# Performance work log

Measured on AMD Instinct MI355X. Metric: run time of the kernel, lower is better.

Reference implementation:

```python
import jax, jax.numpy as jnp
import numpy as np

E = 512   # embed_dim
S = 16    # stat_dim
B = 2048  # batch
K = 64    # neighbors


def setup_inputs() -> dict:
    key = jax.random.key(0)
    ks = jax.random.split(key, 12)
    std_s1 = 1.0 / np.sqrt(3 * E + S)
    std_s2 = 1.0 / np.sqrt(E)
    std_p1 = 1.0 / np.sqrt(E + S)
    return {
        "query": jax.random.normal(ks[0], (B, E), jnp.float32),
        "condition": jax.random.normal(ks[1], (B, E), jnp.float32),
        "neighbors": jax.random.normal(ks[2], (B, K, E), jnp.float32),
        "neighbor_stats": jax.random.uniform(ks[3], (B, K, S), jnp.float32),
        # scorer: Linear(3E+S -> E), GELU, Linear(E -> 1)
        "sw1": jax.random.uniform(ks[4], (3 * E + S, E), jnp.float32, -std_s1, std_s1),
        "sb1": jax.random.uniform(ks[5], (E,), jnp.float32, -std_s1, std_s1),
        "sw2": jax.random.uniform(ks[6], (E, 1), jnp.float32, -std_s2, std_s2),
        "sb2": jax.random.uniform(ks[7], (1,), jnp.float32, -std_s2, std_s2),
        "sim_alpha": jnp.float32(1.0),
        # proj: Linear(E+S -> E), GELU, Linear(E -> E)
        "pw1": jax.random.uniform(ks[8], (E + S, E), jnp.float32, -std_p1, std_p1),
        "pb1": jax.random.uniform(ks[9], (E,), jnp.float32, -std_p1, std_p1),
        "pw2": jax.random.uniform(ks[10], (E, E), jnp.float32, -std_s2, std_s2),
        "pb2": jax.random.uniform(ks[11], (E,), jnp.float32, -std_s2, std_s2),
    }


def _gelu(x):
    return jax.nn.gelu(x, approximate=False)  # torch default GELU is exact erf


def reference(query, condition, neighbors, neighbor_stats,
              sw1, sb1, sw2, sb2, sim_alpha, pw1, pb1, pw2, pb2):
    b, k, e = neighbors.shape
    # broadcast query/condition over k and concat -> [B, K, 3E+S]
    q_rep = jnp.broadcast_to(query[:, None, :], (b, k, e))
    c_rep = jnp.broadcast_to(condition[:, None, :], (b, k, e))
    scorer_in = jnp.concatenate([q_rep, c_rep, neighbors, neighbor_stats], axis=-1)
    h = _gelu(scorer_in @ sw1 + sb1)          # dropout is identity in eval
    logits = (h @ sw2 + sb2)[..., 0]           # [B, K]
    sim_scores = neighbor_stats[..., -1]       # stat_dim > 0
    logits = logits + sim_alpha * sim_scores
    attn = jax.nn.softmax(logits, axis=-1)     # [B, K]
    nb_cat = jnp.concatenate([neighbors, neighbor_stats], axis=-1)  # [B, K, E+S]
    mixed = jnp.einsum('bk,bkd->bd', attn, nb_cat)
    out = _gelu(mixed @ pw1 + pb1) @ pw2 + pb2  # [B, E]
    return out, attn
```

## Files before the change

kernel.cpp:

```cpp
#include <hip/hip_runtime.h>

typedef _Float16 half_t;
typedef _Float16 half2_t __attribute__((ext_vector_type(2)));
typedef _Float16 half4_t __attribute__((ext_vector_type(4)));
typedef _Float16 half8_t __attribute__((ext_vector_type(8)));
typedef float floatx4 __attribute__((ext_vector_type(4)));
typedef float floatx16 __attribute__((ext_vector_type(16)));

#define NE 512
#define NS 16
#define NBATCH 2048
#define NK 64
#define AS 552

__device__ __forceinline__ float gelu_erf(float x) {
    float z = x * 0.70710678118654752440f;
    float az2 = z * z;
    float az = __builtin_fabsf(z);
    float t = __builtin_amdgcn_rcpf(__builtin_fmaf(0.3275911f, az, 1.0f));
    float p = __builtin_fmaf(1.061405429f, t, -1.453152027f);
    p = __builtin_fmaf(p, t, 1.421413741f);
    p = __builtin_fmaf(p, t, -0.284496736f);
    p = __builtin_fmaf(p, t, 0.254829592f);
    p = p * t;
    float e = __expf(-az2);
    float erfa = __builtin_fmaf(-p, e, 1.0f);
    unsigned int u = __float_as_uint(erfa) ^ (__float_as_uint(z) & 0x80000000u);
    return 0.5f * x * (1.0f + __uint_as_float(u));
}

__device__ __forceinline__ half4_t cvt4(float4 v) {
    return (half4_t){(half_t)v.x, (half_t)v.y, (half_t)v.z, (half_t)v.w};
}

__device__ __forceinline__ float colreduce16(const float (&x)[16], int lnb) {
    float y[8];
#pragma unroll
    for (int i = 0; i < 8; ++i) {
        float keep = (lnb & 1) ? x[2 * i + 1] : x[2 * i];
        float send = (lnb & 1) ? x[2 * i] : x[2 * i + 1];
        y[i] = keep + __shfl_xor(send, 1, 64);
    }
    float z[4];
#pragma unroll
    for (int i = 0; i < 4; ++i) {
        float keep = (lnb & 2) ? y[2 * i + 1] : y[2 * i];
        float send = (lnb & 2) ? y[2 * i] : y[2 * i + 1];
        z[i] = keep + __shfl_xor(send, 2, 64);
    }
    float u[2];
#pragma unroll
    for (int i = 0; i < 2; ++i) {
        float keep = (lnb & 4) ? z[2 * i + 1] : z[2 * i];
        float send = (lnb & 4) ? z[2 * i] : z[2 * i + 1];
        u[i] = keep + __shfl_xor(send, 4, 64);
    }
    float keep = (lnb & 8) ? u[1] : u[0];
    float send = (lnb & 8) ? u[0] : u[1];
    float v = keep + __shfl_xor(send, 8, 64);
    v += __shfl_xor(v, 16, 64);
    return v;
}

__device__ void pack_w_body(const float* __restrict__ src, half_t* __restrict__ dst,
                            int Ksrc, int t, int nb0, half_t* tile) {
    int tid = threadIdx.x;
#pragma unroll
    for (int i = 0; i < 8; ++i) {
        int idx = tid + i * 256;
        int kk = idx >> 6, np = idx & 63;
        int k = t * 32 + kk;
        float v = (k < Ksrc) ? src[(size_t)k * NE + nb0 + np] : 0.0f;
        tile[kk * 68 + np] = (half_t)v;
    }
    __syncthreads();
#pragma unroll
    for (int i = 0; i < 8; ++i) {
        int idx = tid + i * 256;
        int np = idx >> 5, kk = idx & 31;
        dst[((size_t)t * NE + nb0 + np) * 32 + kk] = tile[kk * 68 + np];
    }
}

__device__ void pack_w32_body(const float* __restrict__ src, half_t* __restrict__ dst,
                              int Ksrc, int t, int nb0, half_t* tile) {
    int tid = threadIdx.x;
#pragma unroll
    for (int i = 0; i < 4; ++i) {
        int idx = tid + i * 256;
        int kk = idx >> 6, n = idx & 63;
        int k = t * 16 + kk;
        float v = (k < Ksrc) ? src[(size_t)k * NE + nb0 + n] : 0.0f;
        tile[kk * 68 + n] = (half_t)v;
    }
    __syncthreads();
    int n = threadIdx.x >> 2, q = threadIdx.x & 3;
    half4_t h = {tile[(q * 4) * 68 + n], tile[(q * 4 + 1) * 68 + n],
                 tile[(q * 4 + 2) * 68 + n], tile[(q * 4 + 3) * 68 + n]};
    *(half4_t*)&dst[((size_t)t * NE + nb0 + n) * 16 + q * 4] = h;
}

__global__ __launch_bounds__(256) void pack_all(
    const float* __restrict__ sw1, const float* __restrict__ pw1,
    const float* __restrict__ pw2, half_t* __restrict__ Wq,
    half_t* __restrict__ Wns, half_t* __restrict__ Wp1, half_t* __restrict__ Wp2) {
    __shared__ half_t tile[32 * 68];
    int bx = blockIdx.x;
    if (bx < 256) {
        pack_w_body(sw1, Wq, 1024, bx >> 3, (bx & 7) * 64, tile);
    } else if (bx < 520) {
        int b2 = bx - 256;
        pack_w32_body(sw1 + (size_t)1024 * NE, Wns, 528, b2 >> 3, (b2 & 7) * 64, tile);
    } else if (bx < 656) {
        int b3 = bx - 520;
        pack_w_body(pw1, Wp1, 528, b3 >> 3, (b3 & 7) * 64, tile);
    } else {
        int b4 = bx - 656;
        pack_w_body(pw2, Wp2, 512, b4 >> 3, (b4 & 7) * 64, tile);
    }
}

__global__ __launch_bounds__(512) void qc_kernel(const float* __restrict__ q,
                                                 const float* __restrict__ c,
                                                 const half_t* __restrict__ Wq,
                                                 const float* __restrict__ sb1,
                                                 float* __restrict__ qcb) {
    constexpr int AS1 = 1032;
    __shared__ __align__(16) half_t A1[16 * AS1];
    int b0 = (blockIdx.x >> 1) * 16;
    int nh = (blockIdx.x & 1) * 256;
    int tid = threadIdx.x;
#pragma unroll
    for (int i = 0; i < 8; ++i) {
        int f = tid + i * 512;
        int row = f >> 8;
        int c4 = f & 255;
        const float* srcp = (c4 < 128) ? (q + (size_t)(b0 + row) * NE + c4 * 4)
                                       : (c + (size_t)(b0 + row) * NE + (c4 - 128) * 4);
        float4 v = *(const float4*)srcp;
        *(half4_t*)&A1[row * AS1 + c4 * 4] = cvt4(v);
    }
    __syncthreads();
    int w = tid >> 6, l = tid & 63, lg = l >> 4, ln = l & 15;
    floatx4 acc[2] = { {0,0,0,0}, {0,0,0,0} };
    for (int t = 0; t < 32; ++t) {
        half8_t a = *(const half8_t*)&A1[ln * AS1 + t * 32 + 8 * lg];
#pragma unroll
        for (int ni = 0; ni < 2; ++ni) {
            int n = nh + w * 32 + ni * 16 + ln;
            half8_t bf = *(const half8_t*)(Wq + ((size_t)t * NE + n) * 32 + 8 * lg);
            acc[ni] = __builtin_amdgcn_mfma_f32_16x16x32_f16(a, bf, acc[ni], 0, 0, 0);
        }
    }
#pragma unroll
    for (int ni = 0; ni < 2; ++ni) {
        int col = nh + w * 32 + ni * 16 + ln;
        float bias = sb1[col];
#pragma unroll
        for (int r = 0; r < 4; ++r) {
            int row = 4 * lg + r;
            qcb[(size_t)(b0 + row) * NE + col] = acc[ni][r] + bias;
        }
    }
}

__global__ __launch_bounds__(512, 4) void main_kernel(
    const float* __restrict__ neighbors, const float* __restrict__ stats,
    const half_t* __restrict__ Wns, const float* __restrict__ qcb,
    const float* __restrict__ sw2, const float* __restrict__ sb2,
    const float* __restrict__ alpha, float* __restrict__ attn_out,
    half_t* __restrict__ mixed) {
    __shared__ __align__(16) half_t A[64 * AS];
    __shared__ float Llds[64][17];
    __shared__ float attn_s[8][64];

    int b = blockIdx.x;
    int tid = threadIdx.x;
    const float* nb = neighbors + (size_t)b * NK * NE;
    const float* st = stats + (size_t)b * NK * NS;

    int r0 = tid >> 5;
    int c4 = tid & 31;
    int w = tid >> 6;
    int l = tid & 63, ln = l & 31, hi = l >> 5;
    const half_t* Abase = A + ln * AS + 8 * hi;
    const half_t* WbA = Wns + ((size_t)(w * 64 + ln)) * 16 + 8 * hi;
    const half_t* WbB = WbA + 32 * 16;

    float4 s0, s1, s2, s3;
    float qvA, wA, qvB, wB;
    half8_t bfA[4], bfB[4];

    {
        float4 p0 = *(const float4*)(nb + (size_t)(r0) * NE + 4 * c4);
        float4 p1 = *(const float4*)(nb + (size_t)(r0 + 16) * NE + 4 * c4);
        float4 p2 = *(const float4*)(nb + (size_t)(r0 + 32) * NE + 4 * c4);
        float4 p3 = *(const float4*)(nb + (size_t)(r0 + 48) * NE + 4 * c4);
        qvA = qcb[(size_t)b * NE + w * 64 + ln];
        wA = sw2[w * 64 + ln];
        qvB = qcb[(size_t)b * NE + w * 64 + 32 + ln];
        wB = sw2[w * 64 + 32 + ln];
#pragma unroll
        for (int s = 0; s < 4; ++s) {
            bfA[s] = *(const half8_t*)(WbA + (size_t)s * 8192);
            bfB[s] = *(const half8_t*)(WbB + (size_t)s * 8192);
        }
        __builtin_amdgcn_sched_barrier(0);
        *(half4_t*)&A[(r0) * AS + 4 * c4] = cvt4(p0);
        *(half4_t*)&A[(r0 + 16) * AS + 4 * c4] = cvt4(p1);
        *(half4_t*)&A[(r0 + 32) * AS + 4 * c4] = cvt4(p2);
        *(half4_t*)&A[(r0 + 48) * AS + 4 * c4] = cvt4(p3);
    }
    asm volatile("s_waitcnt lgkmcnt(0)" ::: "memory");
    __builtin_amdgcn_sched_barrier(0);
    __builtin_amdgcn_s_barrier();
    __builtin_amdgcn_sched_barrier(0);

    floatx16 acc00 = {0,0,0,0,0,0,0,0,0,0,0,0,0,0,0,0};
    floatx16 acc01 = {0,0,0,0,0,0,0,0,0,0,0,0,0,0,0,0};
    floatx16 acc10 = {0,0,0,0,0,0,0,0,0,0,0,0,0,0,0,0};
    floatx16 acc11 = {0,0,0,0,0,0,0,0,0,0,0,0,0,0,0,0};

#pragma unroll 1
    for (int ch = 0; ch < 3; ++ch) {
        s0 = *(const float4*)(nb + (size_t)(r0) * NE + (ch + 1) * 128 + 4 * c4);
        s1 = *(const float4*)(nb + (size_t)(r0 + 16) * NE + (ch + 1) * 128 + 4 * c4);
        s2 = *(const float4*)(nb + (size_t)(r0 + 32) * NE + (ch + 1) * 128 + 4 * c4);
        s3 = *(const float4*)(nb + (size_t)(r0 + 48) * NE + (ch + 1) * 128 + 4 * c4);
        __builtin_amdgcn_sched_barrier(0);
#pragma unroll
        for (int s8 = 0; s8 < 8; ++s8) {
            const int slot = s8 & 3;
            half8_t bA = bfA[slot], bB = bfB[slot];
            bfA[slot] = *(const half8_t*)(WbA + (size_t)(ch * 8 + s8 + 4) * 8192);
            bfB[slot] = *(const half8_t*)(WbB + (size_t)(ch * 8 + s8 + 4) * 8192);
            int col = ch * 128 + s8 * 16;
            half8_t a0 = *(const half8_t*)&Abase[col];
            half8_t a1 = *(const half8_t*)&Abase[32 * AS + col];
            acc00 = __builtin_amdgcn_mfma_f32_32x32x16_f16(a0, bA, acc00, 0, 0, 0);
            acc10 = __builtin_amdgcn_mfma_f32_32x32x16_f16(a1, bA, acc10, 0, 0, 0);
            acc01 = __builtin_amdgcn_mfma_f32_32x32x16_f16(a0, bB, acc01, 0, 0, 0);
            acc11 = __builtin_amdgcn_mfma_f32_32x32x16_f16(a1, bB, acc11, 0, 0, 0);
        }
        __builtin_amdgcn_sched_barrier(0);
        *(half4_t*)&A[(r0) * AS + (ch + 1) * 128 + 4 * c4] = cvt4(s0);
        *(half4_t*)&A[(r0 + 16) * AS + (ch + 1) * 128 + 4 * c4] = cvt4(s1);
        *(half4_t*)&A[(r0 + 32) * AS + (ch + 1) * 128 + 4 * c4] = cvt4(s2);
        *(half4_t*)&A[(r0 + 48) * AS + (ch + 1) * 128 + 4 * c4] = cvt4(s3);
        asm volatile("s_waitcnt lgkmcnt(0)" ::: "memory");
        __builtin_amdgcn_sched_barrier(0);
        __builtin_amdgcn_s_barrier();
        __builtin_amdgcn_sched_barrier(0);
    }

    {
        if (tid < 256)
            s0 = *(const float4*)(st + (tid >> 2) * NS + (tid & 3) * 4);
        __builtin_amdgcn_sched_barrier(0);
#pragma unroll
        for (int s8 = 0; s8 < 8; ++s8) {
            const int slot = s8 & 3;
            half8_t bA = bfA[slot], bB = bfB[slot];
            if (s8 <= 4) {
                bfA[slot] = *(const half8_t*)(WbA + (size_t)(28 + s8) * 8192);
                bfB[slot] = *(const half8_t*)(WbB + (size_t)(28 + s8) * 8192);
            }
            int col = 3 * 128 + s8 * 16;
            half8_t a0 = *(const half8_t*)&Abase[col];
            half8_t a1 = *(const half8_t*)&Abase[32 * AS + col];
            acc00 = __builtin_amdgcn_mfma_f32_32x32x16_f16(a0, bA, acc00, 0, 0, 0);
            acc10 = __builtin_amdgcn_mfma_f32_32x32x16_f16(a1, bA, acc10, 0, 0, 0);
            acc01 = __builtin_amdgcn_mfma_f32_32x32x16_f16(a0, bB, acc01, 0, 0, 0);
            acc11 = __builtin_amdgcn_mfma_f32_32x32x16_f16(a1, bB, acc11, 0, 0, 0);
        }
        __builtin_amdgcn_sched_barrier(0);
        if (tid < 256)
            *(half4_t*)&A[(tid >> 2) * AS + 512 + (tid & 3) * 4] = cvt4(s0);
        asm volatile("s_waitcnt lgkmcnt(0)" ::: "memory");
        __builtin_amdgcn_sched_barrier(0);
        __builtin_amdgcn_s_barrier();
        __builtin_amdgcn_sched_barrier(0);
    }
    {
        half8_t a0 = *(const half8_t*)&Abase[512];
        half8_t a1 = *(const half8_t*)&Abase[32 * AS + 512];
        acc00 = __builtin_amdgcn_mfma_f32_32x32x16_f16(a0, bfA[0], acc00, 0, 0, 0);
        acc10 = __builtin_amdgcn_mfma_f32_32x32x16_f16(a1, bfA[0], acc10, 0, 0, 0);
        acc01 = __builtin_amdgcn_mfma_f32_32x32x16_f16(a0, bfB[0], acc01, 0, 0, 0);
        acc11 = __builtin_amdgcn_mfma_f32_32x32x16_f16(a1, bfB[0], acc11, 0, 0, 0);
    }

    {
        float g0[16];
#pragma unroll
        for (int r = 0; r < 16; ++r) g0[r] = gelu_erf(acc00[r] + qvA) * wA;
        float rA = colreduce16(g0, ln);
#pragma unroll
        for (int r = 0; r < 16; ++r) g0[r] = gelu_erf(acc01[r] + qvB) * wB;
        float rB = colreduce16(g0, ln);
        if (ln < 16) {
            int row = (ln & 3) + 8 * (ln >> 2) + 4 * hi;
            Llds[row][2 * w] = rA;
            Llds[row][2 * w + 1] = rB;
        }
#pragma unroll
        for (int r = 0; r < 16; ++r) g0[r] = gelu_erf(acc10[r] + qvA) * wA;
        rA = colreduce16(g0, ln);
#pragma unroll
        for (int r = 0; r < 16; ++r) g0[r] = gelu_erf(acc11[r] + qvB) * wB;
        rB = colreduce16(g0, ln);
        if (ln < 16) {
            int row = (ln & 3) + 8 * (ln >> 2) + 4 * hi;
            Llds[32 + row][2 * w] = rA;
            Llds[32 + row][2 * w + 1] = rB;
        }
    }
    __syncthreads();

    {
        int k = l;
        float lsum = 0.0f;
#pragma unroll
        for (int j = 0; j < 16; ++j) lsum += Llds[k][j];
        float sim = st[k * NS + (NS - 1)];
        float logit = lsum + sb2[0] + alpha[0] * sim;
        float mx = logit;
#pragma unroll
        for (int m = 1; m < 64; m <<= 1) mx = fmaxf(mx, __shfl_xor(mx, m, 64));
        float e = __expf(logit - mx);
        float s = e;
#pragma unroll
        for (int m = 1; m < 64; m <<= 1) s += __shfl_xor(s, m, 64);
        float at = e / s;
        attn_s[w][k] = at;
        if (w == 0) attn_out[(size_t)b * NK + k] = at;
    }

    if (tid < 264) {
        int c0 = 2 * tid;
        float m0 = 0.0f, m1 = 0.0f;
#pragma unroll 8
        for (int k = 0; k < NK; ++k) {
            half2_t v = *(const half2_t*)&A[k * AS + c0];
            float aw = attn_s[w][k];
            m0 += aw * (float)v[0];
            m1 += aw * (float)v[1];
        }
        *(half2_t*)&mixed[(size_t)b * AS + c0] = (half2_t){(half_t)m0, (half_t)m1};
    } else if (tid < 270) {
        int z = tid - 264;
        half4_t hz = {};
        *(half4_t*)&mixed[(size_t)b * AS + 528 + 4 * z] = hz;
    }
}

__global__ __launch_bounds__(1024) void proj_kernel(
    const half_t* __restrict__ mixedp, const half_t* __restrict__ Wp1,
    const half_t* __restrict__ Wp2, const float* __restrict__ pb1,
    const float* __restrict__ pb2, float* __restrict__ out) {
    constexpr int AS3 = AS;
    __shared__ __align__(16) half_t A1[16 * AS3];
    int b0 = blockIdx.x * 16;
    int tid = threadIdx.x;
    const uint4* src = (const uint4*)(mixedp + (size_t)b0 * AS3);
    for (int i = tid; i < 1104; i += 1024) ((uint4*)A1)[i] = src[i];
    __syncthreads();

    int w = tid >> 6, l = tid & 63, lg = l >> 4, ln = l & 15;
    floatx4 acc[2] = { {0,0,0,0}, {0,0,0,0} };
    for (int t = 0; t < 17; ++t) {
        half8_t a = *(const half8_t*)&A1[ln * AS3 + t * 32 + 8 * lg];
#pragma unroll
        for (int ni = 0; ni < 2; ++ni) {
            int n = w * 32 + ni * 16 + ln;
            half8_t bf = *(const half8_t*)(Wp1 + ((size_t)t * NE + n) * 32 + 8 * lg);
            acc[ni] = __builtin_amdgcn_mfma_f32_16x16x32_f16(a, bf, acc[ni], 0, 0, 0);
        }
    }
    __syncthreads();
#pragma unroll
    for (int ni = 0; ni < 2; ++ni) {
        int col = w * 32 + ni * 16 + ln;
        float bias = pb1[col];
#pragma unroll
        for (int r = 0; r < 4; ++r) {
            int row = 4 * lg + r;
            A1[row * AS3 + col] = (half_t)gelu_erf(acc[ni][r] + bias);
        }
    }
    __syncthreads();
    floatx4 acc2[2] = { {0,0,0,0}, {0,0,0,0} };
    for (int t = 0; t < 16; ++t) {
        half8_t a = *(const half8_t*)&A1[ln * AS3 + t * 32 + 8 * lg];
#pragma unroll
        for (int ni = 0; ni < 2; ++ni) {
            int n = w * 32 + ni * 16 + ln;
            half8_t bf = *(const half8_t*)(Wp2 + ((size_t)t * NE + n) * 32 + 8 * lg);
            acc2[ni] = __builtin_amdgcn_mfma_f32_16x16x32_f16(a, bf, acc2[ni], 0, 0, 0);
        }
    }
#pragma unroll
    for (int ni = 0; ni < 2; ++ni) {
        int col = w * 32 + ni * 16 + ln;
        float bias = pb2[col];
#pragma unroll
        for (int r = 0; r < 4; ++r)
            out[(size_t)(b0 + 4 * lg + r) * NE + col] = acc2[ni][r] + bias;
    }
}

extern "C" void kernel_launch(void* const* d_in, const int* in_sizes, int n_in,
                              void* d_out, int out_size, void* d_ws, size_t ws_size,
                              hipStream_t stream) {
    (void)in_sizes; (void)n_in; (void)out_size; (void)ws_size;
    const float* q     = (const float*)d_in[0];
    const float* c     = (const float*)d_in[1];
    const float* nb    = (const float*)d_in[2];
    const float* st    = (const float*)d_in[3];
    const float* sw1   = (const float*)d_in[4];
    const float* sb1   = (const float*)d_in[5];
    const float* sw2   = (const float*)d_in[6];
    const float* sb2   = (const float*)d_in[7];
    const float* alpha = (const float*)d_in[8];
    const float* pw1   = (const float*)d_in[9];
    const float* pb1   = (const float*)d_in[10];
    const float* pw2   = (const float*)d_in[11];
    const float* pb2   = (const float*)d_in[12];

    char* ws = (char*)d_ws;
    half_t* Wq  = (half_t*)(ws + 0);
    half_t* Wns = (half_t*)(ws + 1048576);
    half_t* Wp1 = (half_t*)(ws + 1605632);
    half_t* Wp2 = (half_t*)(ws + 2162688);
    float*  qcb = (float*)(ws + 2686976);
    half_t* mix = (half_t*)(ws + 6881280);

    float* outp  = (float*)d_out;
    float* attnp = outp + (size_t)NBATCH * NE;

    pack_all<<<784, 256, 0, stream>>>(sw1, pw1, pw2, Wq, Wns, Wp1, Wp2);
    qc_kernel<<<256, 512, 0, stream>>>(q, c, Wq, sb1, qcb);
    main_kernel<<<2048, 512, 0, stream>>>(nb, st, Wns, qcb, sw2, sb2, alpha, attnp, mix);
    proj_kernel<<<128, 1024, 0, stream>>>(mix, Wp1, Wp2, pb1, pb2, outp);
}
```

Baseline: 182.6 us.

## Halve main_kernel block to 4 waves, each covering 128 hidden columns

Restructures main_kernel from 512 threads (8 waves, 64 hidden columns each) to 256 threads (4 waves, 128 columns each). Each wave now reuses every A-fragment LDS read across 8 MFMAs instead of 4, and double-buffers weight fragments in two register sets. Neighbor chunks are prefetched two chunks ahead with wider per-thread loads, and the stats chunk is folded into the main loop. This cuts LDS traffic per MFMA but doubles accumulator registers and lowers launch occupancy, which reduces latency hiding. The mixed-sum tail is redistributed so 256 threads cover 528 columns.

```diff
diff --git a/kernel.cpp b/kernel.cpp
--- a/kernel.cpp
+++ b/kernel.cpp
@@ -60,6 +60,19 @@
     float v = keep + __shfl_xor(send, 8, 64);
     v += __shfl_xor(v, 16, 64);
     return v;
+}
+
+__device__ __forceinline__ void epi_one(const floatx16& acc, float qv, float w2,
+                                        int rowofs, int cg, int ln, int hi,
+                                        float (*Llds)[17]) {
+    float g[16];
+#pragma unroll
+    for (int r = 0; r < 16; ++r) g[r] = gelu_erf(acc[r] + qv) * w2;
+    float rr = colreduce16(g, ln);
+    if (ln < 16) {
+        int row = (ln & 3) + 8 * (ln >> 2) + 4 * hi;
+        Llds[rowofs + row][cg] = rr;
+    }
 }
 
 __device__ void pack_w_body(const float* __restrict__ src, half_t* __restrict__ dst,
@@ -164,7 +177,7 @@
     }
 }
 
-__global__ __launch_bounds__(512, 4) void main_kernel(
+__global__ __launch_bounds__(256, 2) void main_kernel(
     const float* __restrict__ neighbors, const float* __restrict__ stats,
     const half_t* __restrict__ Wns, const float* __restrict__ qcb,
     const float* __restrict__ sw2, const float* __restrict__ sb2,
@@ -172,44 +185,67 @@
     half_t* __restrict__ mixed) {
     __shared__ __align__(16) half_t A[64 * AS];
     __shared__ float Llds[64][17];
-    __shared__ float attn_s[8][64];
+    __shared__ float attn_s[4][64];
 
     int b = blockIdx.x;
     int tid = threadIdx.x;
     const float* nb = neighbors + (size_t)b * NK * NE;
     const float* st = stats + (size_t)b * NK * NS;
 
-    int r0 = tid >> 5;
-    int c4 = tid & 31;
+    int r0 = tid >> 4;
+    int c4 = tid & 15;
     int w = tid >> 6;
     int l = tid & 63, ln = l & 31, hi = l >> 5;
     const half_t* Abase = A + ln * AS + 8 * hi;
-    const half_t* WbA = Wns + ((size_t)(w * 64 + ln)) * 16 + 8 * hi;
-    const half_t* WbB = WbA + 32 * 16;
-
-    float4 s0, s1, s2, s3;
-    float qvA, wA, qvB, wB;
-    half8_t bfA[4], bfB[4];
+    const half_t* Wb = Wns + ((size_t)(w * 128 + ln)) * 16 + 8 * hi;
+
+    float4 s0, s1, s2, s3, s4, s5, s6, s7;
+    float qv0, qv1, qv2, qv3, w20, w21, w22, w23;
+    half8_t bx0, bx1, bx2, bx3, by0, by1, by2, by3;
 
     {
         float4 p0 = *(const float4*)(nb + (size_t)(r0) * NE + 4 * c4);
         float4 p1 = *(const float4*)(nb + (size_t)(r0 + 16) * NE + 4 * c4);
         float4 p2 = *(const float4*)(nb + (size_t)(r0 + 32) * NE + 4 * c4);
         float4 p3 = *(const float4*)(nb + (size_t)(r0 + 48) * NE + 4 * c4);
-        qvA = qcb[(size_t)b * NE + w * 64 + ln];
-        wA = sw2[w * 64 + ln];
-        qvB = qcb[(size_t)b * NE + w * 64 + 32 + ln];
-        wB = sw2[w * 64 + 32 + ln];
-#pragma unroll
-        for (int s = 0; s < 4; ++s) {
-            bfA[s] = *(const half8_t*)(WbA + (size_t)s * 8192);
-            bfB[s] = *(const half8_t*)(WbB + (size_t)s * 8192);
-        }
+        float4 p4 = *(const float4*)(nb + (size_t)(r0) * NE + 64 + 4 * c4);
+        float4 p5 = *(const float4*)(nb + (size_t)(r0 + 16) * NE + 64 + 4 * c4);
+        float4 p6 = *(const float4*)(nb + (size_t)(r0 + 32) * NE + 64 + 4 * c4);
+        float4 p7 = *(const float4*)(nb + (size_t)(r0 + 48) * NE + 64 + 4 * c4);
+        qv0 = qcb[(size_t)b * NE + w * 128 + ln];
+        qv1 = qcb[(size_t)b * NE + w * 128 + 32 + ln];
+        qv2 = qcb[(size_t)b * NE + w * 128 + 64 + ln];
+        qv3 = qcb[(size_t)b * NE + w * 128 + 96 + ln];
+        w20 = sw2[w * 128 + ln];
+        w21 = sw2[w * 128 + 32 + ln];
+        w22 = sw2[w * 128 + 64 + ln];
+        w23 = sw2[w * 128 + 96 + ln];
+        bx0 = *(const half8_t*)(Wb);
+        bx1 = *(const half8_t*)(Wb + 512);
+        bx2 = *(const half8_t*)(Wb + 1024);
+        bx3 = *(const half8_t*)(Wb + 1536);
+        by0 = *(const half8_t*)(Wb + 8192);
+        by1 = *(const half8_t*)(Wb + 8192 + 512);
+        by2 = *(const half8_t*)(Wb + 8192 + 1024);
+        by3 = *(const half8_t*)(Wb + 8192 + 1536);
         __builtin_amdgcn_sched_barrier(0);
         *(half4_t*)&A[(r0) * AS + 4 * c4] = cvt4(p0);
         *(half4_t*)&A[(r0 + 16) * AS + 4 * c4] = cvt4(p1);
         *(half4_t*)&A[(r0 + 32) * AS + 4 * c4] = cvt4(p2);
         *(half4_t*)&A[(r0 + 48) * AS + 4 * c4] = cvt4(p3);
+        *(half4_t*)&A[(r0) * AS + 64 + 4 * c4] = cvt4(p4);
+        *(half4_t*)&A[(r0 + 16) * AS + 64 + 4 * c4] = cvt4(p5);
+        *(half4_t*)&A[(r0 + 32) * AS + 64 + 4 * c4] = cvt4(p6);
+        *(half4_t*)&A[(r0 + 48) * AS + 64 + 4 * c4] = cvt4(p7);
+        __builtin_amdgcn_sched_barrier(0);
+        s0 = *(const float4*)(nb + (size_t)(r0) * NE + 128 + 4 * c4);
+        s1 = *(const float4*)(nb + (size_t)(r0 + 16) * NE + 128 + 4 * c4);
+        s2 = *(const float4*)(nb + (size_t)(r0 + 32) * NE + 128 + 4 * c4);
+        s3 = *(const float4*)(nb + (size_t)(r0 + 48) * NE + 128 + 4 * c4);
+        s4 = *(const float4*)(nb + (size_t)(r0) * NE + 192 + 4 * c4);
+        s5 = *(const float4*)(nb + (size_t)(r0 + 16) * NE + 192 + 4 * c4);
+        s6 = *(const float4*)(nb + (size_t)(r0 + 32) * NE + 192 + 4 * c4);
+        s7 = *(const float4*)(nb + (size_t)(r0 + 48) * NE + 192 + 4 * c4);
     }
     asm volatile("s_waitcnt lgkmcnt(0)" ::: "memory");
     __builtin_amdgcn_sched_barrier(0);
@@ -218,103 +254,112 @@
 
     floatx16 acc00 = {0,0,0,0,0,0,0,0,0,0,0,0,0,0,0,0};
     floatx16 acc01 = {0,0,0,0,0,0,0,0,0,0,0,0,0,0,0,0};
+    floatx16 acc02 = {0,0,0,0,0,0,0,0,0,0,0,0,0,0,0,0};
+    floatx16 acc03 = {0,0,0,0,0,0,0,0,0,0,0,0,0,0,0,0};
     floatx16 acc10 = {0,0,0,0,0,0,0,0,0,0,0,0,0,0,0,0};
     floatx16 acc11 = {0,0,0,0,0,0,0,0,0,0,0,0,0,0,0,0};
+    floatx16 acc12 = {0,0,0,0,0,0,0,0,0,0,0,0,0,0,0,0};
+    floatx16 acc13 = {0,0,0,0,0,0,0,0,0,0,0,0,0,0,0,0};
 
 #pragma unroll 1
-    for (int ch = 0; ch < 3; ++ch) {
-        s0 = *(const float4*)(nb + (size_t)(r0) * NE + (ch + 1) * 128 + 4 * c4);
-        s1 = *(const float4*)(nb + (size_t)(r0 + 16) * NE + (ch + 1) * 128 + 4 * c4);
-        s2 = *(const float4*)(nb + (size_t)(r0 + 32) * NE + (ch + 1) * 128 + 4 * c4);
-        s3 = *(const float4*)(nb + (size_t)(r0 + 48) * NE + (ch + 1) * 128 + 4 * c4);
+    for (int ch = 0; ch < 4; ++ch) {
+#pragma unroll
+        for (int s2i = 0; s2i < 4; ++s2i) {
+            {
+                int te = ch * 8 + 2 * s2i;
+                int col = te * 16;
+                half8_t a0 = *(const half8_t*)&Abase[col];
+                half8_t a1 = *(const half8_t*)&Abase[32 * AS + col];
+                acc00 = __builtin_amdgcn_mfma_f32_32x32x16_f16(a0, bx0, acc00, 0, 0, 0);
+                acc10 = __builtin_amdgcn_mfma_f32_32x32x16_f16(a1, bx0, acc10, 0, 0, 0);
+                acc01 = __builtin_amdgcn_mfma_f32_32x32x16_f16(a0, bx1, acc01, 0, 0, 0);
+                acc11 = __builtin_amdgcn_mfma_f32_32x32x16_f16(a1, bx1, acc11, 0, 0, 0);
+                acc02 = __builtin_amdgcn_mfma_f32_32x32x16_f16(a0, bx2, acc02, 0, 0, 0);
+                acc12 = __builtin_amdgcn_mfma_f32_32x32x16_f16(a1, bx2, acc12, 0, 0, 0);
+                acc03 = __builtin_amdgcn_mfma_f32_32x32x16_f16(a0, bx3, acc03, 0, 0, 0);
+                acc13 = __builtin_amdgcn_mfma_f32_32x32x16_f16(a1, bx3, acc13, 0, 0, 0);
+                int tn = te + 2; if (tn > 32) tn = 32;
+                const half_t* Wt = Wb + (size_t)tn * 8192;
+                bx0 = *(const half8_t*)(Wt);
+                bx1 = *(const half8_t*)(Wt + 512);
+                bx2 = *(const half8_t*)(Wt + 1024);
+                bx3 = *(const half8_t*)(Wt + 1536);
+            }
+            {
+                int to = ch * 8 + 2 * s2i + 1;
+                int col = to * 16;
+                half8_t a0 = *(const half8_t*)&Abase[col];
+                half8_t a1 = *(const half8_t*)&Abase[32 * AS + col];
+                acc00 = __builtin_amdgcn_mfma_f32_32x32x16_f16(a0, by0, acc00, 0, 0, 0);
+                acc10 = __builtin_amdgcn_mfma_f32_32x32x16_f16(a1, by0, acc10, 0, 0, 0);
+                acc01 = __builtin_amdgcn_mfma_f32_32x32x16_f16(a0, by1, acc01, 0, 0, 0);
+                acc11 = __builtin_amdgcn_mfma_f32_32x32x16_f16(a1, by1, acc11, 0, 0, 0);
+                acc02 = __builtin_amdgcn_mfma_f32_32x32x16_f16(a0, by2, acc02, 0, 0, 0);
+                acc12 = __builtin_amdgcn_mfma_f32_32x32x16_f16(a1, by2, acc12, 0, 0, 0);
+                acc03 = __builtin_amdgcn_mfma_f32_32x32x16_f16(a0, by3, acc03, 0, 0, 0);
+                acc13 = __builtin_amdgcn_mfma_f32_32x32x16_f16(a1, by3, acc13, 0, 0, 0);
+                int tn = to + 2; if (tn > 32) tn = 32;
+                const half_t* Wt = Wb + (size_t)tn * 8192;
+                by0 = *(const half8_t*)(Wt);
+                by1 = *(const half8_t*)(Wt + 512);
+                by2 = *(const half8_t*)(Wt + 1024);
+                by3 = *(const half8_t*)(Wt + 1536);
+            }
+        }
         __builtin_amdgcn_sched_barrier(0);
-#pragma unroll
-        for (int s8 = 0; s8 < 8; ++s8) {
-            const int slot = s8 & 3;
-            half8_t bA = bfA[slot], bB = bfB[slot];
-            bfA[slot] = *(const half8_t*)(WbA + (size_t)(ch * 8 + s8 + 4) * 8192);
-            bfB[slot] = *(const half8_t*)(WbB + (size_t)(ch * 8 + s8 + 4) * 8192);
-            int col = ch * 128 + s8 * 16;
-            half8_t a0 = *(const half8_t*)&Abase[col];
-            half8_t a1 = *(const half8_t*)&Abase[32 * AS + col];
-            acc00 = __builtin_amdgcn_mfma_f32_32x32x16_f16(a0, bA, acc00, 0, 0, 0);
-            acc10 = __builtin_amdgcn_mfma_f32_32x32x16_f16(a1, bA, acc10, 0, 0, 0);
-            acc01 = __builtin_amdgcn_mfma_f32_32x32x16_f16(a0, bB, acc01, 0, 0, 0);
-            acc11 = __builtin_amdgcn_mfma_f32_32x32x16_f16(a1, bB, acc11, 0, 0, 0);
-        }
-        __builtin_amdgcn_sched_barrier(0);
-        *(half4_t*)&A[(r0) * AS + (ch + 1) * 128 + 4 * c4] = cvt4(s0);
-        *(half4_t*)&A[(r0 + 16) * AS + (ch + 1) * 128 + 4 * c4] = cvt4(s1);
-        *(half4_t*)&A[(r0 + 32) * AS + (ch + 1) * 128 + 4 * c4] = cvt4(s2);
-        *(half4_t*)&A[(r0 + 48) * AS + (ch + 1) * 128 + 4 * c4] = cvt4(s3);
+        if (ch < 3) {
+            int cb = (ch + 1) * 128;
+            *(half4_t*)&A[(r0) * AS + cb + 4 * c4] = cvt4(s0);
+            *(half4_t*)&A[(r0 + 16) * AS + cb + 4 * c4] = cvt4(s1);
+            *(half4_t*)&A[(r0 + 32) * AS + cb + 4 * c4] = cvt4(s2);
+            *(half4_t*)&A[(r0 + 48) * AS + cb + 4 * c4] = cvt4(s3);
+            *(half4_t*)&A[(r0) * AS + cb + 64 + 4 * c4] = cvt4(s4);
+            *(half4_t*)&A[(r0 + 16) * AS + cb + 64 + 4 * c4] = cvt4(s5);
+            *(half4_t*)&A[(r0 + 32) * AS + cb + 64 + 4 * c4] = cvt4(s6);
+            *(half4_t*)&A[(r0 + 48) * AS + cb + 64 + 4 * c4] = cvt4(s7);
+            __builtin_amdgcn_sched_barrier(0);
+            if (ch < 2) {
+                int nc = (ch + 2) * 128;
+                s0 = *(const float4*)(nb + (size_t)(r0) * NE + nc + 4 * c4);
+                s1 = *(const float4*)(nb + (size_t)(r0 + 16) * NE + nc + 4 * c4);
+                s2 = *(const float4*)(nb + (size_t)(r0 + 32) * NE + nc + 4 * c4);
+                s3 = *(const float4*)(nb + (size_t)(r0 + 48) * NE + nc + 4 * c4);
+                s4 = *(const float4*)(nb + (size_t)(r0) * NE + nc + 64 + 4 * c4);
+                s5 = *(const float4*)(nb + (size_t)(r0 + 16) * NE + nc + 64 + 4 * c4);
+                s6 = *(const float4*)(nb + (size_t)(r0 + 32) * NE + nc + 64 + 4 * c4);
+                s7 = *(const float4*)(nb + (size_t)(r0 + 48) * NE + nc + 64 + 4 * c4);
+            } else {
+                s0 = *(const float4*)(st + (tid >> 2) * NS + (tid & 3) * 4);
+            }
+        } else {
+            *(half4_t*)&A[(tid >> 2) * AS + 512 + (tid & 3) * 4] = cvt4(s0);
+        }
         asm volatile("s_waitcnt lgkmcnt(0)" ::: "memory");
         __builtin_amdgcn_sched_barrier(0);
         __builtin_amdgcn_s_barrier();
         __builtin_amdgcn_sched_barrier(0);
     }
-
-    {
-        if (tid < 256)
-            s0 = *(const float4*)(st + (tid >> 2) * NS + (tid & 3) * 4);
-        __builtin_amdgcn_sched_barrier(0);
-#pragma unroll
-        for (int s8 = 0; s8 < 8; ++s8) {
-            const int slot = s8 & 3;
-            half8_t bA = bfA[slot], bB = bfB[slot];
-            if (s8 <= 4) {
-                bfA[slot] = *(const half8_t*)(WbA + (size_t)(28 + s8) * 8192);
-                bfB[slot] = *(const half8_t*)(WbB + (size_t)(28 + s8) * 8192);
-            }
-            int col = 3 * 128 + s8 * 16;
-            half8_t a0 = *(const half8_t*)&Abase[col];
-            half8_t a1 = *(const half8_t*)&Abase[32 * AS + col];
-            acc00 = __builtin_amdgcn_mfma_f32_32x32x16_f16(a0, bA, acc00, 0, 0, 0);
-            acc10 = __builtin_amdgcn_mfma_f32_32x32x16_f16(a1, bA, acc10, 0, 0, 0);
-            acc01 = __builtin_amdgcn_mfma_f32_32x32x16_f16(a0, bB, acc01, 0, 0, 0);
-            acc11 = __builtin_amdgcn_mfma_f32_32x32x16_f16(a1, bB, acc11, 0, 0, 0);
-        }
-        __builtin_amdgcn_sched_barrier(0);
-        if (tid < 256)
-            *(half4_t*)&A[(tid >> 2) * AS + 512 + (tid & 3) * 4] = cvt4(s0);
-        asm volatile("s_waitcnt lgkmcnt(0)" ::: "memory");
-        __builtin_amdgcn_sched_barrier(0);
-        __builtin_amdgcn_s_barrier();
-        __builtin_amdgcn_sched_barrier(0);
-    }
     {
         half8_t a0 = *(const half8_t*)&Abase[512];
         half8_t a1 = *(const half8_t*)&Abase[32 * AS + 512];
-        acc00 = __builtin_amdgcn_mfma_f32_32x32x16_f16(a0, bfA[0], acc00, 0, 0, 0);
-        acc10 = __builtin_amdgcn_mfma_f32_32x32x16_f16(a1, bfA[0], acc10, 0, 0, 0);
-        acc01 = __builtin_amdgcn_mfma_f32_32x32x16_f16(a0, bfB[0], acc01, 0, 0, 0);
-        acc11 = __builtin_amdgcn_mfma_f32_32x32x16_f16(a1, bfB[0], acc11, 0, 0, 0);
-    }
-
-    {
-        float g0[16];
-#pragma unroll
-        for (int r = 0; r < 16; ++r) g0[r] = gelu_erf(acc00[r] + qvA) * wA;
-        float rA = colreduce16(g0, ln);
-#pragma unroll
-        for (int r = 0; r < 16; ++r) g0[r] = gelu_erf(acc01[r] + qvB) * wB;
-        float rB = colreduce16(g0, ln);
-        if (ln < 16) {
-            int row = (ln & 3) + 8 * (ln >> 2) + 4 * hi;
-            Llds[row][2 * w] = rA;
-            Llds[row][2 * w + 1] = rB;
-        }
-#pragma unroll
-        for (int r = 0; r < 16; ++r) g0[r] = gelu_erf(acc10[r] + qvA) * wA;
-        rA = colreduce16(g0, ln);
-#pragma unroll
-        for (int r = 0; r < 16; ++r) g0[r] = gelu_erf(acc11[r] + qvB) * wB;
-        rB = colreduce16(g0, ln);
-        if (ln < 16) {
-            int row = (ln & 3) + 8 * (ln >> 2) + 4 * hi;
-            Llds[32 + row][2 * w] = rA;
-            Llds[32 + row][2 * w + 1] = rB;
-        }
-    }
+        acc00 = __builtin_amdgcn_mfma_f32_32x32x16_f16(a0, bx0, acc00, 0, 0, 0);
+        acc10 = __builtin_amdgcn_mfma_f32_32x32x16_f16(a1, bx0, acc10, 0, 0, 0);
+        acc01 = __builtin_amdgcn_mfma_f32_32x32x16_f16(a0, bx1, acc01, 0, 0, 0);
+        acc11 = __builtin_amdgcn_mfma_f32_32x32x16_f16(a1, bx1, acc11, 0, 0, 0);
+        acc02 = __builtin_amdgcn_mfma_f32_32x32x16_f16(a0, bx2, acc02, 0, 0, 0);
+        acc12 = __builtin_amdgcn_mfma_f32_32x32x16_f16(a1, bx2, acc12, 0, 0, 0);
+        acc03 = __builtin_amdgcn_mfma_f32_32x32x16_f16(a0, bx3, acc03, 0, 0, 0);
+        acc13 = __builtin_amdgcn_mfma_f32_32x32x16_f16(a1, bx3, acc13, 0, 0, 0);
+    }
+
+    epi_one(acc00, qv0, w20, 0,  4 * w + 0, ln, hi, Llds);
+    epi_one(acc01, qv1, w21, 0,  4 * w + 1, ln, hi, Llds);
+    epi_one(acc02, qv2, w22, 0,  4 * w + 2, ln, hi, Llds);
+    epi_one(acc03, qv3, w23, 0,  4 * w + 3, ln, hi, Llds);
+    epi_one(acc10, qv0, w20, 32, 4 * w + 0, ln, hi, Llds);
+    epi_one(acc11, qv1, w21, 32, 4 * w + 1, ln, hi, Llds);
+    epi_one(acc12, qv2, w22, 32, 4 * w + 2, ln, hi, Llds);
+    epi_one(acc13, qv3, w23, 32, 4 * w + 3, ln, hi, Llds);
     __syncthreads();
 
     {
@@ -336,7 +381,7 @@
         if (w == 0) attn_out[(size_t)b * NK + k] = at;
     }
 
-    if (tid < 264) {
+    {
         int c0 = 2 * tid;
         float m0 = 0.0f, m1 = 0.0f;
 #pragma unroll 8
@@ -347,10 +392,22 @@
             m1 += aw * (float)v[1];
         }
         *(half2_t*)&mixed[(size_t)b * AS + c0] = (half2_t){(half_t)m0, (half_t)m1};
-    } else if (tid < 270) {
-        int z = tid - 264;
-        half4_t hz = {};
-        *(half4_t*)&mixed[(size_t)b * AS + 528 + 4 * z] = hz;
+        if (tid < 8) {
+            int cs = 512 + 2 * tid;
+            float n0 = 0.0f, n1 = 0.0f;
+#pragma unroll 8
+            for (int k = 0; k < NK; ++k) {
+                half2_t v = *(const half2_t*)&A[k * AS + cs];
+                float aw = attn_s[0][k];
+                n0 += aw * (float)v[0];
+                n1 += aw * (float)v[1];
+            }
+            *(half2_t*)&mixed[(size_t)b * AS + cs] = (half2_t){(half_t)n0, (half_t)n1};
+        } else if (tid < 14) {
+            int z = tid - 8;
+            half4_t hz = {};
+            *(half4_t*)&mixed[(size_t)b * AS + 528 + 4 * z] = hz;
+        }
     }
 }
 
@@ -440,6 +497,6 @@
 
     pack_all<<<784, 256, 0, stream>>>(sw1, pw1, pw2, Wq, Wns, Wp1, Wp2);
     qc_kernel<<<256, 512, 0, stream>>>(q, c, Wq, sb1, qcb);
-    main_kernel<<<2048, 512, 0, stream>>>(nb, st, Wns, qcb, sw2, sb2, alpha, attnp, mix);
+    main_kernel<<<2048, 256, 0, stream>>>(nb, st, Wns, qcb, sw2, sb2, alpha, attnp, mix);
     proj_kernel<<<128, 1024, 0, stream>>>(mix, Wp1, Wp2, pb1, pb2, outp);
 }
```

After: 179.4 us. No clear change (-1.8%).

## Process two batch rows per block to share scorer weight fragments

Applied to the files above, without the earlier changes.

The main kernel now handles two batch elements per 1024-thread block. Each wave owns 32 hidden columns across 128 neighbor rows instead of 64 columns across 64 rows, so every loaded weight fragment feeds four MFMAs over more rows and per-block weight traffic is halved. The neighbor prefetch is deepened by one chunk, MFMA sections get raised wave priority, and the sim stat is staged in LDS. The cost is LDS use of roughly 150KB per block and more register pressure, which limits occupancy to one block per CU. The mixing epilogue also drops from half2 to scalar LDS reads.

```diff
diff --git a/kernel.cpp b/kernel.cpp
--- a/kernel.cpp
+++ b/kernel.cpp
@@ -60,6 +60,19 @@
     float v = keep + __shfl_xor(send, 8, 64);
     v += __shfl_xor(v, 16, 64);
     return v;
+}
+
+__device__ __forceinline__ void epi_one(const floatx16& acc, float qv, float w2,
+                                        int rowofs, int cg, int ln, int hi,
+                                        float (*Llds)[17]) {
+    float g[16];
+#pragma unroll
+    for (int r = 0; r < 16; ++r) g[r] = gelu_erf(acc[r] + qv) * w2;
+    float rr = colreduce16(g, ln);
+    if (ln < 16) {
+        int row = (ln & 3) + 8 * (ln >> 2) + 4 * hi;
+        Llds[rowofs + row][cg] = rr;
+    }
 }
 
 __device__ void pack_w_body(const float* __restrict__ src, half_t* __restrict__ dst,
@@ -164,89 +177,114 @@
     }
 }
 
-__global__ __launch_bounds__(512, 4) void main_kernel(
+__global__ __launch_bounds__(1024, 4) void main_kernel(
     const float* __restrict__ neighbors, const float* __restrict__ stats,
     const half_t* __restrict__ Wns, const float* __restrict__ qcb,
     const float* __restrict__ sw2, const float* __restrict__ sb2,
     const float* __restrict__ alpha, float* __restrict__ attn_out,
     half_t* __restrict__ mixed) {
-    __shared__ __align__(16) half_t A[64 * AS];
-    __shared__ float Llds[64][17];
-    __shared__ float attn_s[8][64];
-
-    int b = blockIdx.x;
+    __shared__ __align__(16) half_t A[128 * AS];
+    __shared__ float Llds[128][17];
+    __shared__ float attn_s[16][64];
+
+    int b0 = blockIdx.x * 2;
     int tid = threadIdx.x;
-    const float* nb = neighbors + (size_t)b * NK * NE;
-    const float* st = stats + (size_t)b * NK * NS;
+    const float* nb0 = neighbors + (size_t)b0 * NK * NE;
+    const float* st0 = stats + (size_t)b0 * NK * NS;
 
     int r0 = tid >> 5;
     int c4 = tid & 31;
     int w = tid >> 6;
     int l = tid & 63, ln = l & 31, hi = l >> 5;
     const half_t* Abase = A + ln * AS + 8 * hi;
-    const half_t* WbA = Wns + ((size_t)(w * 64 + ln)) * 16 + 8 * hi;
-    const half_t* WbB = WbA + 32 * 16;
-
-    float4 s0, s1, s2, s3;
-    float qvA, wA, qvB, wB;
-    half8_t bfA[4], bfB[4];
+    const half_t* Wb = Wns + ((size_t)(w * 32 + ln)) * 16 + 8 * hi;
+
+    float4 s0, s1, s2, s3, sst;
+    float qv0, qv1, w2s;
+    half8_t bf0, bf1, bf2, bf3;
 
     {
-        float4 p0 = *(const float4*)(nb + (size_t)(r0) * NE + 4 * c4);
-        float4 p1 = *(const float4*)(nb + (size_t)(r0 + 16) * NE + 4 * c4);
-        float4 p2 = *(const float4*)(nb + (size_t)(r0 + 32) * NE + 4 * c4);
-        float4 p3 = *(const float4*)(nb + (size_t)(r0 + 48) * NE + 4 * c4);
-        qvA = qcb[(size_t)b * NE + w * 64 + ln];
-        wA = sw2[w * 64 + ln];
-        qvB = qcb[(size_t)b * NE + w * 64 + 32 + ln];
-        wB = sw2[w * 64 + 32 + ln];
-#pragma unroll
-        for (int s = 0; s < 4; ++s) {
-            bfA[s] = *(const half8_t*)(WbA + (size_t)s * 8192);
-            bfB[s] = *(const half8_t*)(WbB + (size_t)s * 8192);
-        }
+        float4 p0 = *(const float4*)(nb0 + (size_t)(r0) * NE + 4 * c4);
+        float4 p1 = *(const float4*)(nb0 + (size_t)(r0 + 32) * NE + 4 * c4);
+        float4 p2 = *(const float4*)(nb0 + (size_t)(r0 + 64) * NE + 4 * c4);
+        float4 p3 = *(const float4*)(nb0 + (size_t)(r0 + 96) * NE + 4 * c4);
+        qv0 = qcb[(size_t)b0 * NE + w * 32 + ln];
+        qv1 = qcb[(size_t)(b0 + 1) * NE + w * 32 + ln];
+        w2s = sw2[w * 32 + ln];
+        bf0 = *(const half8_t*)(Wb);
+        bf1 = *(const half8_t*)(Wb + 8192);
+        bf2 = *(const half8_t*)(Wb + 2 * 8192);
+        bf3 = *(const half8_t*)(Wb + 3 * 8192);
         __builtin_amdgcn_sched_barrier(0);
         *(half4_t*)&A[(r0) * AS + 4 * c4] = cvt4(p0);
-        *(half4_t*)&A[(r0 + 16) * AS + 4 * c4] = cvt4(p1);
-        *(half4_t*)&A[(r0 + 32) * AS + 4 * c4] = cvt4(p2);
-        *(half4_t*)&A[(r0 + 48) * AS + 4 * c4] = cvt4(p3);
+        *(half4_t*)&A[(r0 + 32) * AS + 4 * c4] = cvt4(p1);
+        *(half4_t*)&A[(r0 + 64) * AS + 4 * c4] = cvt4(p2);
+        *(half4_t*)&A[(r0 + 96) * AS + 4 * c4] = cvt4(p3);
+        __builtin_amdgcn_sched_barrier(0);
+        s0 = *(const float4*)(nb0 + (size_t)(r0) * NE + 128 + 4 * c4);
+        s1 = *(const float4*)(nb0 + (size_t)(r0 + 32) * NE + 128 + 4 * c4);
+        s2 = *(const float4*)(nb0 + (size_t)(r0 + 64) * NE + 128 + 4 * c4);
+        s3 = *(const float4*)(nb0 + (size_t)(r0 + 96) * NE + 128 + 4 * c4);
+        if (tid < 128) Llds[tid][16] = st0[tid * NS + (NS - 1)];
     }
     asm volatile("s_waitcnt lgkmcnt(0)" ::: "memory");
     __builtin_amdgcn_sched_barrier(0);
     __builtin_amdgcn_s_barrier();
     __builtin_amdgcn_sched_barrier(0);
 
-    floatx16 acc00 = {0,0,0,0,0,0,0,0,0,0,0,0,0,0,0,0};
-    floatx16 acc01 = {0,0,0,0,0,0,0,0,0,0,0,0,0,0,0,0};
-    floatx16 acc10 = {0,0,0,0,0,0,0,0,0,0,0,0,0,0,0,0};
-    floatx16 acc11 = {0,0,0,0,0,0,0,0,0,0,0,0,0,0,0,0};
+    floatx16 acc0 = {0,0,0,0,0,0,0,0,0,0,0,0,0,0,0,0};
+    floatx16 acc1 = {0,0,0,0,0,0,0,0,0,0,0,0,0,0,0,0};
+    floatx16 acc2 = {0,0,0,0,0,0,0,0,0,0,0,0,0,0,0,0};
+    floatx16 acc3 = {0,0,0,0,0,0,0,0,0,0,0,0,0,0,0,0};
 
 #pragma unroll 1
     for (int ch = 0; ch < 3; ++ch) {
-        s0 = *(const float4*)(nb + (size_t)(r0) * NE + (ch + 1) * 128 + 4 * c4);
-        s1 = *(const float4*)(nb + (size_t)(r0 + 16) * NE + (ch + 1) * 128 + 4 * c4);
-        s2 = *(const float4*)(nb + (size_t)(r0 + 32) * NE + (ch + 1) * 128 + 4 * c4);
-        s3 = *(const float4*)(nb + (size_t)(r0 + 48) * NE + (ch + 1) * 128 + 4 * c4);
-        __builtin_amdgcn_sched_barrier(0);
+        float4 n0, n1, n2, n3;
+        if (ch < 2) {
+            int nc = (ch + 2) * 128;
+            n0 = *(const float4*)(nb0 + (size_t)(r0) * NE + nc + 4 * c4);
+            n1 = *(const float4*)(nb0 + (size_t)(r0 + 32) * NE + nc + 4 * c4);
+            n2 = *(const float4*)(nb0 + (size_t)(r0 + 64) * NE + nc + 4 * c4);
+            n3 = *(const float4*)(nb0 + (size_t)(r0 + 96) * NE + nc + 4 * c4);
+        } else {
+            if (tid < 512)
+                sst = *(const float4*)(st0 + (tid >> 2) * NS + (tid & 3) * 4);
+        }
+        __builtin_amdgcn_sched_barrier(0);
+        __builtin_amdgcn_s_setprio(1);
 #pragma unroll
         for (int s8 = 0; s8 < 8; ++s8) {
-            const int slot = s8 & 3;
-            half8_t bA = bfA[slot], bB = bfB[slot];
-            bfA[slot] = *(const half8_t*)(WbA + (size_t)(ch * 8 + s8 + 4) * 8192);
-            bfB[slot] = *(const half8_t*)(WbB + (size_t)(ch * 8 + s8 + 4) * 8192);
-            int col = ch * 128 + s8 * 16;
+            int t = ch * 8 + s8;
+            int col = t * 16;
+            half8_t bc;
+            if ((s8 & 3) == 0) bc = bf0;
+            else if ((s8 & 3) == 1) bc = bf1;
+            else if ((s8 & 3) == 2) bc = bf2;
+            else bc = bf3;
             half8_t a0 = *(const half8_t*)&Abase[col];
             half8_t a1 = *(const half8_t*)&Abase[32 * AS + col];
-            acc00 = __builtin_amdgcn_mfma_f32_32x32x16_f16(a0, bA, acc00, 0, 0, 0);
-            acc10 = __builtin_amdgcn_mfma_f32_32x32x16_f16(a1, bA, acc10, 0, 0, 0);
-            acc01 = __builtin_amdgcn_mfma_f32_32x32x16_f16(a0, bB, acc01, 0, 0, 0);
-            acc11 = __builtin_amdgcn_mfma_f32_32x32x16_f16(a1, bB, acc11, 0, 0, 0);
-        }
-        __builtin_amdgcn_sched_barrier(0);
-        *(half4_t*)&A[(r0) * AS + (ch + 1) * 128 + 4 * c4] = cvt4(s0);
-        *(half4_t*)&A[(r0 + 16) * AS + (ch + 1) * 128 + 4 * c4] = cvt4(s1);
-        *(half4_t*)&A[(r0 + 32) * AS + (ch + 1) * 128 + 4 * c4] = cvt4(s2);
-        *(half4_t*)&A[(r0 + 48) * AS + (ch + 1) * 128 + 4 * c4] = cvt4(s3);
+            half8_t a2 = *(const half8_t*)&Abase[64 * AS + col];
+            half8_t a3 = *(const half8_t*)&Abase[96 * AS + col];
+            acc0 = __builtin_amdgcn_mfma_f32_32x32x16_f16(a0, bc, acc0, 0, 0, 0);
+            acc1 = __builtin_amdgcn_mfma_f32_32x32x16_f16(a1, bc, acc1, 0, 0, 0);
+            acc2 = __builtin_amdgcn_mfma_f32_32x32x16_f16(a2, bc, acc2, 0, 0, 0);
+            acc3 = __builtin_amdgcn_mfma_f32_32x32x16_f16(a3, bc, acc3, 0, 0, 0);
+            half8_t nb8 = *(const half8_t*)(Wb + (size_t)(t + 4) * 8192);
+            if ((s8 & 3) == 0) bf0 = nb8;
+            else if ((s8 & 3) == 1) bf1 = nb8;
+            else if ((s8 & 3) == 2) bf2 = nb8;
+            else bf3 = nb8;
+        }
+        __builtin_amdgcn_s_setprio(0);
+        __builtin_amdgcn_sched_barrier(0);
+        {
+            int cb = (ch + 1) * 128;
+            *(half4_t*)&A[(r0) * AS + cb + 4 * c4] = cvt4(s0);
+            *(half4_t*)&A[(r0 + 32) * AS + cb + 4 * c4] = cvt4(s1);
+            *(half4_t*)&A[(r0 + 64) * AS + cb + 4 * c4] = cvt4(s2);
+            *(half4_t*)&A[(r0 + 96) * AS + cb + 4 * c4] = cvt4(s3);
+            s0 = n0; s1 = n1; s2 = n2; s3 = n3;
+        }
         asm volatile("s_waitcnt lgkmcnt(0)" ::: "memory");
         __builtin_amdgcn_sched_barrier(0);
         __builtin_amdgcn_s_barrier();
@@ -254,28 +292,36 @@
     }
 
     {
-        if (tid < 256)
-            s0 = *(const float4*)(st + (tid >> 2) * NS + (tid & 3) * 4);
-        __builtin_amdgcn_sched_barrier(0);
+        __builtin_amdgcn_s_setprio(1);
 #pragma unroll
         for (int s8 = 0; s8 < 8; ++s8) {
-            const int slot = s8 & 3;
-            half8_t bA = bfA[slot], bB = bfB[slot];
-            if (s8 <= 4) {
-                bfA[slot] = *(const half8_t*)(WbA + (size_t)(28 + s8) * 8192);
-                bfB[slot] = *(const half8_t*)(WbB + (size_t)(28 + s8) * 8192);
-            }
-            int col = 3 * 128 + s8 * 16;
+            int t = 24 + s8;
+            int col = t * 16;
+            half8_t bc;
+            if ((s8 & 3) == 0) bc = bf0;
+            else if ((s8 & 3) == 1) bc = bf1;
+            else if ((s8 & 3) == 2) bc = bf2;
+            else bc = bf3;
             half8_t a0 = *(const half8_t*)&Abase[col];
             half8_t a1 = *(const half8_t*)&Abase[32 * AS + col];
-            acc00 = __builtin_amdgcn_mfma_f32_32x32x16_f16(a0, bA, acc00, 0, 0, 0);
-            acc10 = __builtin_amdgcn_mfma_f32_32x32x16_f16(a1, bA, acc10, 0, 0, 0);
-            acc01 = __builtin_amdgcn_mfma_f32_32x32x16_f16(a0, bB, acc01, 0, 0, 0);
-            acc11 = __builtin_amdgcn_mfma_f32_32x32x16_f16(a1, bB, acc11, 0, 0, 0);
-        }
-        __builtin_amdgcn_sched_barrier(0);
-        if (tid < 256)
-            *(half4_t*)&A[(tid >> 2) * AS + 512 + (tid & 3) * 4] = cvt4(s0);
+            half8_t a2 = *(const half8_t*)&Abase[64 * AS + col];
+            half8_t a3 = *(const half8_t*)&Abase[96 * AS + col];
+            acc0 = __builtin_amdgcn_mfma_f32_32x32x16_f16(a0, bc, acc0, 0, 0, 0);
+            acc1 = __builtin_amdgcn_mfma_f32_32x32x16_f16(a1, bc, acc1, 0, 0, 0);
+            acc2 = __builtin_amdgcn_mfma_f32_32x32x16_f16(a2, bc, acc2, 0, 0, 0);
+            acc3 = __builtin_amdgcn_mfma_f32_32x32x16_f16(a3, bc, acc3, 0, 0, 0);
+            if (s8 <= 4) {
+                half8_t nb8 = *(const half8_t*)(Wb + (size_t)(t + 4) * 8192);
+                if ((s8 & 3) == 0) bf0 = nb8;
+                else if ((s8 & 3) == 1) bf1 = nb8;
+                else if ((s8 & 3) == 2) bf2 = nb8;
+                else bf3 = nb8;
+            }
+        }
+        __builtin_amdgcn_s_setprio(0);
+        __builtin_amdgcn_sched_barrier(0);
+        if (tid < 512)
+            *(half4_t*)&A[(tid >> 2) * AS + 512 + (tid & 3) * 4] = cvt4(sst);
         asm volatile("s_waitcnt lgkmcnt(0)" ::: "memory");
         __builtin_amdgcn_sched_barrier(0);
         __builtin_amdgcn_s_barrier();
@@ -284,45 +330,29 @@
     {
         half8_t a0 = *(const half8_t*)&Abase[512];
         half8_t a1 = *(const half8_t*)&Abase[32 * AS + 512];
-        acc00 = __builtin_amdgcn_mfma_f32_32x32x16_f16(a0, bfA[0], acc00, 0, 0, 0);
-        acc10 = __builtin_amdgcn_mfma_f32_32x32x16_f16(a1, bfA[0], acc10, 0, 0, 0);
-        acc01 = __builtin_amdgcn_mfma_f32_32x32x16_f16(a0, bfB[0], acc01, 0, 0, 0);
-        acc11 = __builtin_amdgcn_mfma_f32_32x32x16_f16(a1, bfB[0], acc11, 0, 0, 0);
-    }
+        half8_t a2 = *(const half8_t*)&Abase[64 * AS + 512];
+        half8_t a3 = *(const half8_t*)&Abase[96 * AS + 512];
+        __builtin_amdgcn_s_setprio(1);
+        acc0 = __builtin_amdgcn_mfma_f32_32x32x16_f16(a0, bf0, acc0, 0, 0, 0);
+        acc1 = __builtin_amdgcn_mfma_f32_32x32x16_f16(a1, bf0, acc1, 0, 0, 0);
+        acc2 = __builtin_amdgcn_mfma_f32_32x32x16_f16(a2, bf0, acc2, 0, 0, 0);
+        acc3 = __builtin_amdgcn_mfma_f32_32x32x16_f16(a3, bf0, acc3, 0, 0, 0);
+        __builtin_amdgcn_s_setprio(0);
+    }
+
+    epi_one(acc0, qv0, w2s, 0,  w, ln, hi, Llds);
+    epi_one(acc1, qv0, w2s, 32, w, ln, hi, Llds);
+    epi_one(acc2, qv1, w2s, 64, w, ln, hi, Llds);
+    epi_one(acc3, qv1, w2s, 96, w, ln, hi, Llds);
+    __syncthreads();
 
     {
-        float g0[16];
-#pragma unroll
-        for (int r = 0; r < 16; ++r) g0[r] = gelu_erf(acc00[r] + qvA) * wA;
-        float rA = colreduce16(g0, ln);
-#pragma unroll
-        for (int r = 0; r < 16; ++r) g0[r] = gelu_erf(acc01[r] + qvB) * wB;
-        float rB = colreduce16(g0, ln);
-        if (ln < 16) {
-            int row = (ln & 3) + 8 * (ln >> 2) + 4 * hi;
-            Llds[row][2 * w] = rA;
-            Llds[row][2 * w + 1] = rB;
-        }
-#pragma unroll
-        for (int r = 0; r < 16; ++r) g0[r] = gelu_erf(acc10[r] + qvA) * wA;
-        rA = colreduce16(g0, ln);
-#pragma unroll
-        for (int r = 0; r < 16; ++r) g0[r] = gelu_erf(acc11[r] + qvB) * wB;
-        rB = colreduce16(g0, ln);
-        if (ln < 16) {
-            int row = (ln & 3) + 8 * (ln >> 2) + 4 * hi;
-            Llds[32 + row][2 * w] = rA;
-            Llds[32 + row][2 * w + 1] = rB;
-        }
-    }
-    __syncthreads();
-
-    {
+        int g = w >> 3;
         int k = l;
         float lsum = 0.0f;
 #pragma unroll
-        for (int j = 0; j < 16; ++j) lsum += Llds[k][j];
-        float sim = st[k * NS + (NS - 1)];
+        for (int j = 0; j < 16; ++j) lsum += Llds[g * 64 + k][j];
+        float sim = Llds[g * 64 + k][16];
         float logit = lsum + sb2[0] + alpha[0] * sim;
         float mx = logit;
 #pragma unroll
@@ -333,24 +363,31 @@
         for (int m = 1; m < 64; m <<= 1) s += __shfl_xor(s, m, 64);
         float at = e / s;
         attn_s[w][k] = at;
-        if (w == 0) attn_out[(size_t)b * NK + k] = at;
-    }
-
-    if (tid < 264) {
-        int c0 = 2 * tid;
-        float m0 = 0.0f, m1 = 0.0f;
+        if (w == 0) attn_out[(size_t)b0 * NK + k] = at;
+        if (w == 8) attn_out[(size_t)(b0 + 1) * NK + k] = at;
+    }
+
+    {
+        int g = tid >> 9;
+        int c0 = tid & 511;
+        float m0 = 0.0f;
 #pragma unroll 8
         for (int k = 0; k < NK; ++k) {
-            half2_t v = *(const half2_t*)&A[k * AS + c0];
             float aw = attn_s[w][k];
-            m0 += aw * (float)v[0];
-            m1 += aw * (float)v[1];
-        }
-        *(half2_t*)&mixed[(size_t)b * AS + c0] = (half2_t){(half_t)m0, (half_t)m1};
-    } else if (tid < 270) {
-        int z = tid - 264;
-        half4_t hz = {};
-        *(half4_t*)&mixed[(size_t)b * AS + 528 + 4 * z] = hz;
+            m0 += aw * (float)A[(g * 64 + k) * AS + c0];
+        }
+        mixed[(size_t)(b0 + g) * AS + c0] = (half_t)m0;
+        if (c0 < 16) {
+            int cs = 512 + c0;
+            float n0 = 0.0f;
+#pragma unroll 8
+            for (int k = 0; k < NK; ++k)
+                n0 += attn_s[w][k] * (float)A[(g * 64 + k) * AS + cs];
+            mixed[(size_t)(b0 + g) * AS + cs] = (half_t)n0;
+        } else if (c0 < 28) {
+            int z = c0 - 16;
+            *(half2_t*)&mixed[(size_t)(b0 + g) * AS + 528 + 2 * z] = (half2_t){};
+        }
     }
 }
 
@@ -440,6 +477,6 @@
 
     pack_all<<<784, 256, 0, stream>>>(sw1, pw1, pw2, Wq, Wns, Wp1, Wp2);
     qc_kernel<<<256, 512, 0, stream>>>(q, c, Wq, sb1, qcb);
-    main_kernel<<<2048, 512, 0, stream>>>(nb, st, Wns, qcb, sw2, sb2, alpha, attnp, mix);
+    main_kernel<<<1024, 1024, 0, stream>>>(nb, st, Wns, qcb, sw2, sb2, alpha, attnp, mix);
     proj_kernel<<<128, 1024, 0, stream>>>(mix, Wp1, Wp2, pb1, pb2, outp);
 }
```

Result: slower. 206.5 us (+13.0%).
